# Optimization experiments

Measured on AMD Instinct MI355X. Metric: run time of the kernel, lower is better.

The kernel has to match this reference:

```python
import jax, jax.numpy as jnp
import numpy as np

N = 100_000      # atom_count
E = 6_400_000    # number of (directed) edges, avg degree 64
BOX = 100.0      # simulation box edge length


def setup_inputs() -> dict:
    key = jax.random.key(0)
    k1, k2, k3 = jax.random.split(key, 3)
    pos = jax.random.uniform(k1, (N, 3), dtype=jnp.float32) * BOX
    src = jax.random.randint(k2, (E,), 0, N, dtype=jnp.int32)
    # offset in [1, N) guarantees dst != src (no zero-distance self edges)
    off = jax.random.randint(k3, (E,), 1, N, dtype=jnp.int32)
    dst = ((src + off) % N).astype(jnp.int32)
    edge_index = jnp.stack([src, dst], axis=0)  # [2, E]
    sigma = jnp.asarray(0.3, dtype=jnp.float32)
    epsilon = jnp.asarray(1.0, dtype=jnp.float32)
    return {"pos": pos, "sigma": sigma, "epsilon": epsilon, "edge_index": edge_index}


def _total_energy(pos, sigma, epsilon, src, dst):
    # r = edge_attr: per-edge distance, differentiable w.r.t. pos
    d = pos[src] - pos[dst]                      # [E, 3] gather + subtract
    r = jnp.sqrt(jnp.sum(d * d, axis=-1))        # [E]
    sr6 = (sigma / r) ** 6
    # potential_formula: 4*epsilon*((sigma/r)**12 - (sigma/r)**6)
    v_r = 4.0 * epsilon * (sr6 * sr6 - sr6)      # [E]
    return v_r.sum()


def reference(pos, sigma, epsilon, edge_index):
    src, dst = edge_index[0], edge_index[1]
    energy = _total_energy(pos, sigma, epsilon, src, dst)
    # afc: autograd force — grad of summed pair potential w.r.t. positions
    # (per-edge force scattered onto atoms by edge_index; grad does the
    #  gather-compute-scatter in one pass)
    pair_force = jax.grad(_total_energy, argnums=0)(pos, sigma, epsilon, src, dst)
    atom_force = -pair_force / 2.0               # /2: each pair counted twice
    return energy, atom_force
```

## Files before the change

kernel.cpp:

```cpp
#include <hip/hip_runtime.h>


#define ROW_F   307200

#define NB2     16
#define BA2     6400
#define BF2     (BA2 * 3)
#define KCH     16
#define NSEG    2048
#define SCG     512
#define SCB     512
#define CAP     512

#define NBINS      8
#define BIN_ATOMS  12800
#define BIN_F      (BIN_ATOMS * 3)
#define BLOCK      1024
#define MAXCHUNKS  32

__global__ __launch_bounds__(SCB) void pf_scatter(
    const float* __restrict__ pos,
    float4*      __restrict__ pos4,
    const int*   __restrict__ src,
    const int*   __restrict__ dst,
    unsigned*    __restrict__ buckets,
    unsigned*    __restrict__ cnt,
    int nEdges, int nAtoms)
{
    __shared__ unsigned shcur[4 * NB2];
    const int t = threadIdx.x, lane = t & 63, wv = t >> 6;
    if (t < 4 * NB2) shcur[t] = 0;

    for (int i = blockIdx.x * SCB + t; i < nAtoms; i += SCG * SCB)
        pos4[i] = make_float4(pos[3 * i + 0], pos[3 * i + 1], pos[3 * i + 2], 0.f);

    __syncthreads();

    const int p = blockIdx.x * 8 + wv;
    const int w = p >> 1;
    unsigned* mycur = shcur + (wv >> 1) * NB2;

    const int epw  = ((nEdges + 2 * NSEG - 1) / (2 * NSEG) + 3) & ~3;
    const int ebeg = p * epw;
    const int eend = min(nEdges, ebeg + epw);
    const int i4beg = ebeg >> 2;
    const int i4end = eend >> 2;

    const int4* src4 = (const int4*)src;
    const int4* dst4 = (const int4*)dst;

    int4 s4 = make_int4(0, 0, 0, 0), d4 = make_int4(0, 0, 0, 0);
    {
        const int i4 = i4beg + lane;
        if (i4 < i4end) { s4 = src4[i4]; d4 = dst4[i4]; }
    }
    for (int base = i4beg; base < i4end; base += 64) {
        const int  i4n  = base + 64 + lane;
        const bool actn = i4n < i4end;
        int4 s4n = make_int4(0, 0, 0, 0), d4n = make_int4(0, 0, 0, 0);
        if (actn) { s4n = src4[i4n]; d4n = dst4[i4n]; }
        if (base + lane < i4end) {
            #pragma unroll
            for (int k = 0; k < 4; ++k) {
                const unsigned su = (unsigned)((k == 0) ? s4.x : (k == 1) ? s4.y : (k == 2) ? s4.z : s4.w);
                const unsigned du = (unsigned)((k == 0) ? d4.x : (k == 1) ? d4.y : (k == 2) ? d4.z : d4.w);
                const unsigned sb = su / BA2, db = du / BA2;
                const unsigned recS = ((su - sb * BA2) << 18) | (1u << 17) | du;
                const unsigned recD = ((du - db * BA2) << 18) | su;
                const unsigned is = atomicAdd(&mycur[sb], 1u);
                if (is < CAP) buckets[((size_t)w * NB2 + sb) * CAP + is] = recS;
                const unsigned id = atomicAdd(&mycur[db], 1u);
                if (id < CAP) buckets[((size_t)w * NB2 + db) * CAP + id] = recD;
            }
        }
        s4 = s4n; d4 = d4n;
    }
    __syncthreads();
    if (t < 4 * NB2) {
        const unsigned cv = shcur[t];
        cnt[(blockIdx.x * 4) * NB2 + t] = cv < CAP ? cv : CAP;
    }
}

__global__ __launch_bounds__(1024, 1) void pf_accum(
    const float*    __restrict__ pos,
    const float4*   __restrict__ pos4,
    const float*    __restrict__ sigma_p,
    const float*    __restrict__ eps_p,
    const unsigned* __restrict__ buckets,
    const unsigned* __restrict__ cnt,
    float* __restrict__ frep,
    float* __restrict__ erep,
    int nAtoms)
{
    extern __shared__ float sh[];
    float* shp = sh + BF2 + 16;
    const int t = threadIdx.x, lane = t & 63, v = t >> 6;
    const int b = blockIdx.x / KCH;
    const int c = blockIdx.x % KCH;

    for (int j = t; j < (BF2 + 16) / 4; j += 1024)
        ((float4*)sh)[j] = make_float4(0.f, 0.f, 0.f, 0.f);

    const int binStart = b * BA2;
    const int binCnt   = min(BA2, nAtoms - binStart);
    const int nf       = binCnt * 3;
    const float4* gp   = (const float4*)(pos + (size_t)binStart * 3);
    for (int j = t; j < (nf >> 2); j += 1024) ((float4*)shp)[j] = gp[j];
    for (int j = (nf & ~3) + t; j < nf; j += 1024) shp[j] = pos[binStart * 3 + j];
    __syncthreads();

    const float sigma = sigma_p[0], eps = eps_p[0];
    const float sig2 = sigma * sigma;
    const float c12 = 12.f * eps, c4 = 4.f * eps;

    float ev = 0.f;
    const int slot = c * 16 + v;

    for (int k = 0; k < NSEG / 256; ++k) {
        const int w = slot + (k << 8);
        const int n = cnt[w * NB2 + b];
        const uint4* seg4 = (const uint4*)(buckets + ((size_t)w * NB2 + b) * CAP);
        const int n4 = (n + 3) >> 2;

        uint4 rqA = make_uint4(0u, 0u, 0u, 0u);
        uint4 rqB = make_uint4(0u, 0u, 0u, 0u);
        if (lane < n4)      rqA = seg4[lane];
        if (lane + 64 < n4) rqB = seg4[lane + 64];
        const int baseA = 4 * lane;
        const int baseB = 4 * (lane + 64);

        unsigned rr[8];
        float4   po[8];
        #pragma unroll
        for (int e = 0; e < 8; ++e) {
            const int rb = (e < 4) ? (baseA + e) : (baseB + e - 4);
            unsigned rec = (e == 0) ? rqA.x : (e == 1) ? rqA.y : (e == 2) ? rqA.z :
                           (e == 3) ? rqA.w : (e == 4) ? rqB.x : (e == 5) ? rqB.y :
                           (e == 6) ? rqB.z : rqB.w;
            rec = (rb < n) ? rec : 0u;
            rr[e] = rec;
            po[e] = pos4[rec & 0x1FFFF];
        }
        #pragma unroll
        for (int e = 0; e < 8; ++e) {
            const int rb = (e < 4) ? (baseA + e) : (baseB + e - 4);
            const unsigned rec = rr[e];
            const int la = rec >> 18;
            const float ax = shp[3 * la + 0];
            const float ay = shp[3 * la + 1];
            const float az = shp[3 * la + 2];
            const float dx = ax - po[e].x, dy = ay - po[e].y, dz = az - po[e].z;
            const float r2   = dx * dx + dy * dy + dz * dz;
            const float ir2  = 1.0f / r2;
            const float s2   = sig2 * ir2;
            const float sr6  = s2 * s2 * s2;
            const float sr12 = sr6 * sr6;
            const float fs   = c12 * (2.f * sr12 - sr6) * ir2;
            if (rb < n) {
                atomicAdd(&sh[3 * la + 0], fs * dx);
                atomicAdd(&sh[3 * la + 1], fs * dy);
                atomicAdd(&sh[3 * la + 2], fs * dz);
                ev += (rec & (1u << 17)) ? c4 * (sr12 - sr6) : 0.f;
            }
        }
    }

    #pragma unroll
    for (int off = 32; off > 0; off >>= 1) ev += __shfl_down(ev, off, 64);
    if (lane == 0) sh[BF2 + v] = ev;
    __syncthreads();

    float4* outSeg = (float4*)(frep + (size_t)c * ROW_F + (size_t)b * BF2);
    for (int j = t; j < BF2 / 4; j += 1024) outSeg[j] = ((float4*)sh)[j];

    if (t == 0) {
        float e = 0.f;
        #pragma unroll
        for (int w2 = 0; w2 < 16; ++w2) e += sh[BF2 + w2];
        erep[blockIdx.x] = e;
    }
}

__global__ __launch_bounds__(256) void pairforce_reduce(
    const float* __restrict__ frep,
    const float* __restrict__ erep,
    float* __restrict__ out,
    int n3, int nChunks, int nPart)
{
    const int i = blockIdx.x * 256 + threadIdx.x;
    if (i < n3) {
        float acc = 0.f;
        for (int c = 0; c < nChunks; ++c)
            acc += frep[(size_t)c * ROW_F + i];
        out[1 + i] = acc;
    }
    if (blockIdx.x == gridDim.x - 1) {
        float e = 0.f;
        for (int j = threadIdx.x; j < nPart; j += 256) e += erep[j];
        #pragma unroll
        for (int off = 32; off > 0; off >>= 1) e += __shfl_down(e, off, 64);
        __shared__ float ep[4];
        if ((threadIdx.x & 63) == 0) ep[threadIdx.x >> 6] = e;
        __syncthreads();
        if (threadIdx.x == 0) out[0] = ep[0] + ep[1] + ep[2] + ep[3];
    }
}

__global__ __launch_bounds__(BLOCK, 1) void pairforce_binned(
    const float* __restrict__ pos,
    const float* __restrict__ sigma_p,
    const float* __restrict__ eps_p,
    const int*   __restrict__ src,
    const int*   __restrict__ dst,
    float* __restrict__ frep,
    float* __restrict__ erep,
    int nEdges, int chunkEdges)
{
    extern __shared__ float sh[];
    const int t = threadIdx.x;
    const int b = blockIdx.x % NBINS;
    const int c = blockIdx.x / NBINS;

    for (int j = t; j < (BIN_F + 16) / 4; j += BLOCK)
        ((float4*)sh)[j] = make_float4(0.f, 0.f, 0.f, 0.f);
    __syncthreads();

    const float sigma = sigma_p[0];
    const float eps   = eps_p[0];
    const float sig2  = sigma * sigma;
    const int binStart = b * BIN_ATOMS;

    const int start = c * chunkEdges;
    const int end   = min(start + chunkEdges, nEdges);

    const int4* src4 = (const int4*)src;
    const int4* dst4 = (const int4*)dst;

    float ev = 0.0f;

    for (int i4 = (start >> 2) + t; i4 < (end >> 2); i4 += BLOCK) {
        const int4 s4 = src4[i4];
        const int4 d4 = dst4[i4];
        #pragma unroll
        for (int k = 0; k < 4; ++k) {
            const int s = (k == 0) ? s4.x : (k == 1) ? s4.y : (k == 2) ? s4.z : s4.w;
            const int d = (k == 0) ? d4.x : (k == 1) ? d4.y : (k == 2) ? d4.z : d4.w;
            const unsigned ls = (unsigned)(s - binStart);
            const unsigned ld = (unsigned)(d - binStart);
            const bool hs = ls < BIN_ATOMS;
            const bool hd = ld < BIN_ATOMS;
            if (hs | hd) {
                const float dx = pos[3 * s + 0] - pos[3 * d + 0];
                const float dy = pos[3 * s + 1] - pos[3 * d + 1];
                const float dz = pos[3 * s + 2] - pos[3 * d + 2];
                const float r2     = dx * dx + dy * dy + dz * dz;
                const float inv_r2 = 1.0f / r2;
                const float s2     = sig2 * inv_r2;
                const float sr6    = s2 * s2 * s2;
                const float sr12   = sr6 * sr6;
                const float fs = 12.0f * eps * (2.0f * sr12 - sr6) * inv_r2;
                const float fx = fs * dx;
                const float fy = fs * dy;
                const float fz = fs * dz;
                if (hs) {
                    atomicAdd(&sh[3 * ls + 0],  fx);
                    atomicAdd(&sh[3 * ls + 1],  fy);
                    atomicAdd(&sh[3 * ls + 2],  fz);
                    ev += 4.0f * eps * (sr12 - sr6);
                }
                if (hd) {
                    atomicAdd(&sh[3 * ld + 0], -fx);
                    atomicAdd(&sh[3 * ld + 1], -fy);
                    atomicAdd(&sh[3 * ld + 2], -fz);
                }
            }
        }
    }

    #pragma unroll
    for (int off = 32; off > 0; off >>= 1)
        ev += __shfl_down(ev, off, 64);
    if ((t & 63) == 0) sh[BIN_F + (t >> 6)] = ev;
    __syncthreads();

    float4* outSeg = (float4*)(frep + (size_t)c * ROW_F + (size_t)b * BIN_F);
    for (int j = t; j < BIN_F / 4; j += BLOCK)
        outSeg[j] = ((float4*)sh)[j];

    if (t == 0) {
        float e = 0.f;
        #pragma unroll
        for (int w = 0; w < 16; ++w) e += sh[BIN_F + w];
        erep[blockIdx.x] = e;
    }
}

extern "C" void kernel_launch(void* const* d_in, const int* in_sizes, int n_in,
                              void* d_out, int out_size, void* d_ws, size_t ws_size,
                              hipStream_t stream)
{
    const float* pos     = (const float*)d_in[0];
    const float* sigma_p = (const float*)d_in[1];
    const float* eps_p   = (const float*)d_in[2];
    const int*   edge    = (const int*)d_in[3];

    const int nEdges = in_sizes[3] / 2;
    const int* src = edge;
    const int* dst = edge + nEdges;

    const int n3 = out_size - 1;
    const int nAtoms = n3 / 3;

    size_t off = 0;
    float*    pos4    = (float*)d_ws;                    off += (size_t)(NB2 * BA2) * 16;
    unsigned* buckets = (unsigned*)((char*)d_ws + off);  off += (size_t)NSEG * NB2 * CAP * 4;
    unsigned* cntp    = (unsigned*)((char*)d_ws + off);  off += (size_t)NSEG * NB2 * 4;
    float*    frepN   = (float*)((char*)d_ws + off);     off += (size_t)KCH * ROW_F * 4;
    float*    erepN   = (float*)((char*)d_ws + off);     off += 256 * 4;

    if (ws_size >= off && nAtoms <= NB2 * BA2 && (nEdges & 3) == 0) {
        pf_scatter<<<SCG, SCB, 0, stream>>>(pos, (float4*)pos4, src, dst,
                                            buckets, cntp, nEdges, nAtoms);
        const size_t shb = (size_t)(BF2 + 16 + BF2) * sizeof(float);
        pf_accum<<<NB2 * KCH, 1024, shb, stream>>>(pos, (const float4*)pos4,
                                                   sigma_p, eps_p, buckets, cntp,
                                                   frepN, erepN, nAtoms);
        pairforce_reduce<<<(n3 + 255) / 256, 256, 0, stream>>>(
            frepN, erepN, (float*)d_out, n3, KCH, NB2 * KCH);
        return;
    }

    const size_t rowBytes = (size_t)ROW_F * sizeof(float);
    int nChunks = (int)((ws_size - 4096) / rowBytes);
    if (nChunks > MAXCHUNKS) nChunks = MAXCHUNKS;
    if (nChunks < 1) nChunks = 1;

    const int chunkEdges = (((nEdges + nChunks - 1) / nChunks) + 3) & ~3;

    float* frep = (float*)d_ws;
    float* erep = frep + (size_t)nChunks * ROW_F;

    const size_t shbytes = (size_t)(BIN_F + 16) * sizeof(float);

    const int grid1 = nChunks * NBINS;
    pairforce_binned<<<grid1, BLOCK, shbytes, stream>>>(
        pos, sigma_p, eps_p, src, dst, frep, erep, nEdges, chunkEdges);

    const int grid2 = (n3 + 255) / 256;
    pairforce_reduce<<<grid2, 256, 0, stream>>>(
        frep, erep, (float*)d_out, n3, nChunks, nChunks * NBINS);
}
```

Before: 342.8 us.

## Split accumulation bins into halves and widen scatter with non-temporal loads

The accumulate kernel now launches two blocks per bin, one per half of the bin's atoms. Each block keeps only its half of positions and forces in LDS and skips records that target the other half, which halves LDS use and allows more resident blocks. The scatter kernel doubles its grid, shares each bucket counter among four waves instead of two, and reads edge and bucket streams with non-temporal loads through workgroup-scoped atomics. In exchange, every block still reads all bucket records and gathers positions even for records it then discards. A new guard on atom count restricts the fast path to inputs that nearly fill all 16 bins.

```diff
diff --git a/kernel.cpp b/kernel.cpp
--- a/kernel.cpp
+++ b/kernel.cpp
@@ -5,10 +5,11 @@
 
 #define NB2     16
 #define BA2     6400
-#define BF2     (BA2 * 3)
+#define HALF_A  3200
+#define HF      (HALF_A * 3)
 #define KCH     16
 #define NSEG    2048
-#define SCG     512
+#define SCG     1024
 #define SCB     512
 #define CAP     512
 
@@ -18,7 +19,23 @@
 #define BLOCK      1024
 #define MAXCHUNKS  32
 
-__global__ __launch_bounds__(SCB) void pf_scatter(
+typedef __attribute__((ext_vector_type(4))) unsigned uvec4;
+typedef __attribute__((ext_vector_type(4))) int      ivec4;
+
+__device__ __forceinline__ uvec4 nt_load_u4(const unsigned* p) {
+    return __builtin_nontemporal_load((const uvec4*)p);
+}
+__device__ __forceinline__ ivec4 nt_load_i4(const int* p) {
+    return __builtin_nontemporal_load((const ivec4*)p);
+}
+__device__ __forceinline__ void lds_fadd(float* p, float v) {
+    __hip_atomic_fetch_add(p, v, __ATOMIC_RELAXED, __HIP_MEMORY_SCOPE_WORKGROUP);
+}
+__device__ __forceinline__ unsigned lds_uinc(unsigned* p) {
+    return __hip_atomic_fetch_add(p, 1u, __ATOMIC_RELAXED, __HIP_MEMORY_SCOPE_WORKGROUP);
+}
+
+__global__ __launch_bounds__(SCB, 8) void pf_scatter(
     const float* __restrict__ pos,
     float4*      __restrict__ pos4,
     const int*   __restrict__ src,
@@ -27,9 +44,9 @@
     unsigned*    __restrict__ cnt,
     int nEdges, int nAtoms)
 {
-    __shared__ unsigned shcur[4 * NB2];
+    __shared__ unsigned shcur[2 * NB2];
     const int t = threadIdx.x, lane = t & 63, wv = t >> 6;
-    if (t < 4 * NB2) shcur[t] = 0;
+    if (t < 2 * NB2) shcur[t] = 0;
 
     for (int i = blockIdx.x * SCB + t; i < nAtoms; i += SCG * SCB)
         pos4[i] = make_float4(pos[3 * i + 0], pos[3 * i + 1], pos[3 * i + 2], 0.f);
@@ -37,52 +54,48 @@
     __syncthreads();
 
     const int p = blockIdx.x * 8 + wv;
-    const int w = p >> 1;
-    unsigned* mycur = shcur + (wv >> 1) * NB2;
-
-    const int epw  = ((nEdges + 2 * NSEG - 1) / (2 * NSEG) + 3) & ~3;
+    const int w = p >> 2;
+    unsigned* mycur = shcur + (wv >> 2) * NB2;
+
+    const int epw  = ((nEdges + 8 * SCG - 1) / (8 * SCG) + 3) & ~3;
     const int ebeg = p * epw;
     const int eend = min(nEdges, ebeg + epw);
     const int i4beg = ebeg >> 2;
     const int i4end = eend >> 2;
 
-    const int4* src4 = (const int4*)src;
-    const int4* dst4 = (const int4*)dst;
-
-    int4 s4 = make_int4(0, 0, 0, 0), d4 = make_int4(0, 0, 0, 0);
+    ivec4 s4 = (ivec4)0, d4 = (ivec4)0;
     {
         const int i4 = i4beg + lane;
-        if (i4 < i4end) { s4 = src4[i4]; d4 = dst4[i4]; }
+        if (i4 < i4end) { s4 = nt_load_i4(src + 4 * i4); d4 = nt_load_i4(dst + 4 * i4); }
     }
     for (int base = i4beg; base < i4end; base += 64) {
         const int  i4n  = base + 64 + lane;
-        const bool actn = i4n < i4end;
-        int4 s4n = make_int4(0, 0, 0, 0), d4n = make_int4(0, 0, 0, 0);
-        if (actn) { s4n = src4[i4n]; d4n = dst4[i4n]; }
+        ivec4 s4n = (ivec4)0, d4n = (ivec4)0;
+        if (i4n < i4end) { s4n = nt_load_i4(src + 4 * i4n); d4n = nt_load_i4(dst + 4 * i4n); }
         if (base + lane < i4end) {
             #pragma unroll
             for (int k = 0; k < 4; ++k) {
-                const unsigned su = (unsigned)((k == 0) ? s4.x : (k == 1) ? s4.y : (k == 2) ? s4.z : s4.w);
-                const unsigned du = (unsigned)((k == 0) ? d4.x : (k == 1) ? d4.y : (k == 2) ? d4.z : d4.w);
+                const unsigned su = (unsigned)s4[k];
+                const unsigned du = (unsigned)d4[k];
                 const unsigned sb = su / BA2, db = du / BA2;
                 const unsigned recS = ((su - sb * BA2) << 18) | (1u << 17) | du;
                 const unsigned recD = ((du - db * BA2) << 18) | su;
-                const unsigned is = atomicAdd(&mycur[sb], 1u);
+                const unsigned is = lds_uinc(&mycur[sb]);
                 if (is < CAP) buckets[((size_t)w * NB2 + sb) * CAP + is] = recS;
-                const unsigned id = atomicAdd(&mycur[db], 1u);
+                const unsigned id = lds_uinc(&mycur[db]);
                 if (id < CAP) buckets[((size_t)w * NB2 + db) * CAP + id] = recD;
             }
         }
         s4 = s4n; d4 = d4n;
     }
     __syncthreads();
-    if (t < 4 * NB2) {
+    if (t < 2 * NB2) {
         const unsigned cv = shcur[t];
-        cnt[(blockIdx.x * 4) * NB2 + t] = cv < CAP ? cv : CAP;
-    }
-}
-
-__global__ __launch_bounds__(1024, 1) void pf_accum(
+        cnt[(blockIdx.x * 2) * NB2 + t] = cv < CAP ? cv : CAP;
+    }
+}
+
+__global__ __launch_bounds__(1024, 8) void pf_accum(
     const float*    __restrict__ pos,
     const float4*   __restrict__ pos4,
     const float*    __restrict__ sigma_p,
@@ -94,25 +107,28 @@
     int nAtoms)
 {
     extern __shared__ float sh[];
-    float* shp = sh + BF2 + 16;
+    float* shp = sh + HF + 16;
     const int t = threadIdx.x, lane = t & 63, v = t >> 6;
-    const int b = blockIdx.x / KCH;
-    const int c = blockIdx.x % KCH;
-
-    for (int j = t; j < (BF2 + 16) / 4; j += 1024)
+    const int b   = blockIdx.x / (2 * KCH);
+    const int rem = blockIdx.x % (2 * KCH);
+    const int h   = rem / KCH;
+    const int c   = rem % KCH;
+
+    for (int j = t; j < (HF + 16) / 4; j += 1024)
         ((float4*)sh)[j] = make_float4(0.f, 0.f, 0.f, 0.f);
 
-    const int binStart = b * BA2;
-    const int binCnt   = min(BA2, nAtoms - binStart);
-    const int nf       = binCnt * 3;
-    const float4* gp   = (const float4*)(pos + (size_t)binStart * 3);
-    for (int j = t; j < (nf >> 2); j += 1024) ((float4*)shp)[j] = gp[j];
-    for (int j = (nf & ~3) + t; j < nf; j += 1024) shp[j] = pos[binStart * 3 + j];
+    const int aStart = b * BA2 + h * HALF_A;
+    const int hCnt   = min(HALF_A, nAtoms - aStart);
+    const int nf     = hCnt * 3;
+    const float* gp  = pos + (size_t)aStart * 3;
+    for (int j = t; j < (nf >> 2); j += 1024) ((float4*)shp)[j] = ((const float4*)gp)[j];
+    for (int j = (nf & ~3) + t; j < nf; j += 1024) shp[j] = gp[j];
     __syncthreads();
 
     const float sigma = sigma_p[0], eps = eps_p[0];
     const float sig2 = sigma * sigma;
     const float c12 = 12.f * eps, c4 = 4.f * eps;
+    const unsigned lbase = (unsigned)h * HALF_A;
 
     float ev = 0.f;
     const int slot = c * 16 + v;
@@ -120,36 +136,33 @@
     for (int k = 0; k < NSEG / 256; ++k) {
         const int w = slot + (k << 8);
         const int n = cnt[w * NB2 + b];
-        const uint4* seg4 = (const uint4*)(buckets + ((size_t)w * NB2 + b) * CAP);
-        const int n4 = (n + 3) >> 2;
-
-        uint4 rqA = make_uint4(0u, 0u, 0u, 0u);
-        uint4 rqB = make_uint4(0u, 0u, 0u, 0u);
-        if (lane < n4)      rqA = seg4[lane];
-        if (lane + 64 < n4) rqB = seg4[lane + 64];
-        const int baseA = 4 * lane;
-        const int baseB = 4 * (lane + 64);
+        const unsigned* seg = buckets + ((size_t)w * NB2 + b) * CAP;
+
+        const uvec4 rqA = nt_load_u4(seg + 4 * lane);
+        const uvec4 rqB = nt_load_u4(seg + 4 * (lane + 64));
 
         unsigned rr[8];
+        int      ls[8];
+        bool     act[8];
         float4   po[8];
         #pragma unroll
         for (int e = 0; e < 8; ++e) {
-            const int rb = (e < 4) ? (baseA + e) : (baseB + e - 4);
-            unsigned rec = (e == 0) ? rqA.x : (e == 1) ? rqA.y : (e == 2) ? rqA.z :
-                           (e == 3) ? rqA.w : (e == 4) ? rqB.x : (e == 5) ? rqB.y :
-                           (e == 6) ? rqB.z : rqB.w;
-            rec = (rb < n) ? rec : 0u;
-            rr[e] = rec;
-            po[e] = pos4[rec & 0x1FFFF];
+            const int rb = (e < 4) ? (4 * lane + e) : (4 * (lane + 64) + e - 4);
+            unsigned rec = (e < 4) ? rqA[e] : rqB[e - 4];
+            const unsigned l = (rec >> 18) - lbase;
+            const bool a = (rb < n) & (l < (unsigned)HALF_A);
+            act[e] = a;
+            rec    = a ? rec : 0u;
+            rr[e]  = rec;
+            ls[e]  = a ? (int)l : 0;
+            po[e]  = pos4[rec & 0x1FFFF];
         }
         #pragma unroll
         for (int e = 0; e < 8; ++e) {
-            const int rb = (e < 4) ? (baseA + e) : (baseB + e - 4);
-            const unsigned rec = rr[e];
-            const int la = rec >> 18;
-            const float ax = shp[3 * la + 0];
-            const float ay = shp[3 * la + 1];
-            const float az = shp[3 * la + 2];
+            const int  l   = ls[e];
+            const float ax = shp[3 * l + 0];
+            const float ay = shp[3 * l + 1];
+            const float az = shp[3 * l + 2];
             const float dx = ax - po[e].x, dy = ay - po[e].y, dz = az - po[e].z;
             const float r2   = dx * dx + dy * dy + dz * dz;
             const float ir2  = 1.0f / r2;
@@ -157,27 +170,27 @@
             const float sr6  = s2 * s2 * s2;
             const float sr12 = sr6 * sr6;
             const float fs   = c12 * (2.f * sr12 - sr6) * ir2;
-            if (rb < n) {
-                atomicAdd(&sh[3 * la + 0], fs * dx);
-                atomicAdd(&sh[3 * la + 1], fs * dy);
-                atomicAdd(&sh[3 * la + 2], fs * dz);
-                ev += (rec & (1u << 17)) ? c4 * (sr12 - sr6) : 0.f;
+            if (act[e]) {
+                lds_fadd(&sh[3 * l + 0], fs * dx);
+                lds_fadd(&sh[3 * l + 1], fs * dy);
+                lds_fadd(&sh[3 * l + 2], fs * dz);
+                ev += (rr[e] & (1u << 17)) ? c4 * (sr12 - sr6) : 0.f;
             }
         }
     }
 
     #pragma unroll
     for (int off = 32; off > 0; off >>= 1) ev += __shfl_down(ev, off, 64);
-    if (lane == 0) sh[BF2 + v] = ev;
-    __syncthreads();
-
-    float4* outSeg = (float4*)(frep + (size_t)c * ROW_F + (size_t)b * BF2);
-    for (int j = t; j < BF2 / 4; j += 1024) outSeg[j] = ((float4*)sh)[j];
+    if (lane == 0) sh[HF + v] = ev;
+    __syncthreads();
+
+    float4* outSeg = (float4*)(frep + (size_t)c * ROW_F + (size_t)aStart * 3);
+    for (int j = t; j < HF / 4; j += 1024) outSeg[j] = ((float4*)sh)[j];
 
     if (t == 0) {
         float e = 0.f;
         #pragma unroll
-        for (int w2 = 0; w2 < 16; ++w2) e += sh[BF2 + w2];
+        for (int w2 = 0; w2 < 16; ++w2) e += sh[HF + w2];
         erep[blockIdx.x] = e;
     }
 }
@@ -317,17 +330,18 @@
     unsigned* buckets = (unsigned*)((char*)d_ws + off);  off += (size_t)NSEG * NB2 * CAP * 4;
     unsigned* cntp    = (unsigned*)((char*)d_ws + off);  off += (size_t)NSEG * NB2 * 4;
     float*    frepN   = (float*)((char*)d_ws + off);     off += (size_t)KCH * ROW_F * 4;
-    float*    erepN   = (float*)((char*)d_ws + off);     off += 256 * 4;
-
-    if (ws_size >= off && nAtoms <= NB2 * BA2 && (nEdges & 3) == 0) {
+    float*    erepN   = (float*)((char*)d_ws + off);     off += (size_t)(NB2 * 2 * KCH) * 4;
+
+    if (ws_size >= off && nAtoms <= NB2 * BA2 && nAtoms > 15 * BA2 + HALF_A &&
+        (nEdges & 3) == 0) {
         pf_scatter<<<SCG, SCB, 0, stream>>>(pos, (float4*)pos4, src, dst,
                                             buckets, cntp, nEdges, nAtoms);
-        const size_t shb = (size_t)(BF2 + 16 + BF2) * sizeof(float);
-        pf_accum<<<NB2 * KCH, 1024, shb, stream>>>(pos, (const float4*)pos4,
-                                                   sigma_p, eps_p, buckets, cntp,
-                                                   frepN, erepN, nAtoms);
+        const size_t shb = (size_t)(HF + 16 + HF) * sizeof(float);
+        pf_accum<<<NB2 * 2 * KCH, 1024, shb, stream>>>(pos, (const float4*)pos4,
+                                                       sigma_p, eps_p, buckets, cntp,
+                                                       frepN, erepN, nAtoms);
         pairforce_reduce<<<(n3 + 255) / 256, 256, 0, stream>>>(
-            frepN, erepN, (float*)d_out, n3, KCH, NB2 * KCH);
+            frepN, erepN, (float*)d_out, n3, KCH, NB2 * 2 * KCH);
         return;
     }
 
```

Result: no change. 341.8 us (-0.3%).
